# Performance work log

Measured on AMD Instinct MI355X. Metric: run time of the kernel, lower is better.

Reference implementation:

```python
import jax, jax.numpy as jnp
import numpy as np

C = 1.0          # Poincare ball curvature
H = 8            # num_heads
EPS = 1e-15
DELTA = 1e-7
SC = np.sqrt(C)  # sqrt curvature


def _norm(x):
    return jnp.sqrt(jnp.clip(jnp.sum(x * x, -1, keepdims=True), 1e-15))


def mobius_add(x, y):
    xy = jnp.sum(x * y, -1, keepdims=True)
    x2 = jnp.sum(x * x, -1, keepdims=True)
    y2 = jnp.sum(y * y, -1, keepdims=True)
    num = (1 + 2 * C * xy + C * y2) * x + (1 - C * x2) * y
    den = 1 + 2 * C * xy + C * C * x2 * y2
    return num / (den + EPS)


def mobius_matvec(W, x):
    xn = _norm(x)
    mx = x @ W.T
    mxn = _norm(mx)
    arg = jnp.clip(SC * xn, None, 1 - 1e-5)
    return jnp.tanh(mxn / xn * jnp.arctanh(arg)) * mx / (mxn * SC)


def logmap0(x):
    xn = _norm(x)
    return jnp.arctanh(jnp.clip(SC * xn, None, 1 - 1e-5)) * x / (SC * xn)


def expmap0(u):
    un = _norm(u)
    return jnp.tanh(SC * un) * u / (SC * un)


def hyp_linear(W, b, x):
    return mobius_add(mobius_matvec(W, x), b)


def setup_inputs() -> dict:
    key = jax.random.key(0)
    ks = jax.random.split(key, 5)
    B, S, E = 2, 512, 256
    x = jax.random.normal(ks[0], (B, S, E), jnp.float32) * 0.02  # inside unit ball
    scale = float(np.sqrt(6.0 / (E + E)))  # xavier uniform bound
    Wq = jax.random.uniform(ks[1], (E, E), jnp.float32, -scale, scale)
    Wk = jax.random.uniform(ks[2], (E, E), jnp.float32, -scale, scale)
    Wv = jax.random.uniform(ks[3], (E, E), jnp.float32, -scale, scale)
    Wo = jax.random.uniform(ks[4], (E, E), jnp.float32, -scale, scale)
    z = jnp.zeros((E,), jnp.float32)
    head_scaling = jnp.ones((H, 1, 1), jnp.float32)
    return {"x": x, "Wq": Wq, "bq": z, "Wk": Wk, "bk": z, "Wv": Wv, "bv": z,
            "Wo": Wo, "bo": z, "head_scaling": head_scaling}


def reference(x, Wq, bq, Wk, bk, Wv, bv, Wo, bo, head_scaling):
    B, S, E = x.shape
    D = E // H
    q = hyp_linear(Wq, bq, x).reshape(B, S, H, D).transpose(0, 2, 1, 3)  # (B,H,S,D)
    k = hyp_linear(Wk, bk, x).reshape(B, S, H, D).transpose(0, 2, 1, 3)
    v = hyp_linear(Wv, bv, x).reshape(B, S, H, D).transpose(0, 2, 1, 3)
    max_norm = (1 - 1e-5) / SC
    q = jnp.minimum(q, max_norm)  # elementwise clamp_max, faithful to source
    k = jnp.minimum(k, max_norm)
    qn = C * jnp.sum(q * q, -1)[..., :, None]   # (B,H,Sq,1)
    kn = C * jnp.sum(k * k, -1)[..., None, :]   # (B,H,1,Sk)
    # pairwise mobius_add(-k, q): (B,H,Sq,Sk,D)
    diff = mobius_add(-k[:, :, None, :, :], q[:, :, :, None, :])
    dn = C * jnp.sum(diff * diff, -1)           # (B,H,Sq,Sk)
    denom = (1 - qn) * (1 - kn) + EPS
    a = jnp.maximum(1 + 2 * dn / denom, 1 + DELTA)
    dist = jnp.log(a + jnp.sqrt(a * a - 1))     # acosh
    scores = -dist / (head_scaling * np.sqrt(D))
    w = jax.nn.softmax(scores, -1)
    out = expmap0(jnp.einsum('bhqk,bhkd->bhqd', w, logmap0(v)))
    out = out.transpose(0, 2, 1, 3).reshape(B, S, E)
    return hyp_linear(Wo, bo, out)
```

## Files before the change

kernel.cpp:

```cpp
#include <hip/hip_runtime.h>
#include <math.h>

#define Ec 256
#define Sc 512
#define Bc 2
#define Hc 8
#define Dc 32
#define MAXNORM (1.0f - 1e-5f)
#define NEc (Bc * Sc * Ec)

__device__ __forceinline__ float fullWaveSum(float v) {
#pragma unroll
  for (int m = 32; m >= 1; m >>= 1) v += __shfl_xor(v, m, 64);
  return v;
}
__device__ __forceinline__ float halfWaveSum(float v) {
#pragma unroll
  for (int m = 16; m >= 1; m >>= 1) v += __shfl_xor(v, m, 64);
  return v;
}
__device__ __forceinline__ float atanh_fast(float z) {
  return 0.5f * __logf((1.0f + z) / (1.0f - z));
}
__device__ __forceinline__ float tanh_fast(float a) {
  float e = __expf(-2.0f * a);
  return (1.0f - e) / (1.0f + e);
}

__global__ __launch_bounds__(128) void gemm_xwt(
    const float* __restrict__ X,
    const float* __restrict__ W0, const float* __restrict__ W1,
    const float* __restrict__ W2,
    float* __restrict__ O0, float* __restrict__ O1, float* __restrict__ O2) {
  const int tid = threadIdx.x;
  const int bx = blockIdx.x;
  const int by = blockIdx.y;
  const int kz = blockIdx.z;
  const int mat = by >> 2;
  const int cb0 = (by & 3) * 64;
  const int rb0 = bx * 32;
  const float* __restrict__ W = (mat == 0) ? W0 : (mat == 1) ? W1 : W2;
  float* __restrict__ O = ((mat == 0) ? O0 : (mat == 1) ? O1 : O2) + (size_t)kz * NEc;

  __shared__ float Xs[64][36];
  __shared__ float Ws[64][68];

  const int f4 = tid & 15;
  const int sub = tid >> 4;
  const int ty = tid >> 4;
  const int tx = tid & 15;

  float acc[4][4];
#pragma unroll
  for (int i = 0; i < 4; ++i)
#pragma unroll
    for (int j = 0; j < 4; ++j) acc[i][j] = 0.f;

  for (int kk = kz * 128; kk < kz * 128 + 128; kk += 64) {
    __syncthreads();
#pragma unroll
    for (int i = 0; i < 4; ++i) {
      int row = sub + i * 8;
      float4 v = *(const float4*)&X[(size_t)(rb0 + row) * Ec + kk + f4 * 4];
      Xs[f4 * 4 + 0][row] = v.x;
      Xs[f4 * 4 + 1][row] = v.y;
      Xs[f4 * 4 + 2][row] = v.z;
      Xs[f4 * 4 + 3][row] = v.w;
    }
#pragma unroll
    for (int i = 0; i < 8; ++i) {
      int col = sub + i * 8;
      float4 v = *(const float4*)&W[(size_t)(cb0 + col) * Ec + kk + f4 * 4];
      Ws[f4 * 4 + 0][col] = v.x;
      Ws[f4 * 4 + 1][col] = v.y;
      Ws[f4 * 4 + 2][col] = v.z;
      Ws[f4 * 4 + 3][col] = v.w;
    }
    __syncthreads();
#pragma unroll 8
    for (int k = 0; k < 64; ++k) {
      float4 a = *(const float4*)&Xs[k][ty * 4];
      float4 b = *(const float4*)&Ws[k][tx * 4];
      float av[4] = {a.x, a.y, a.z, a.w};
      float bv[4] = {b.x, b.y, b.z, b.w};
#pragma unroll
      for (int i = 0; i < 4; ++i)
#pragma unroll
        for (int j = 0; j < 4; ++j) acc[i][j] = fmaf(av[i], bv[j], acc[i][j]);
    }
  }
#pragma unroll
  for (int i = 0; i < 4; ++i) {
    float4 o = make_float4(acc[i][0], acc[i][1], acc[i][2], acc[i][3]);
    *(float4*)&O[(size_t)(rb0 + ty * 4 + i) * Ec + cb0 + tx * 4] = o;
  }
}

__global__ __launch_bounds__(256) void qkv_stats(
    const float* __restrict__ x,
    const float* __restrict__ mxq, const float* __restrict__ mxk,
    const float* __restrict__ mxv,
    const float* __restrict__ bq, const float* __restrict__ bk,
    const float* __restrict__ bv,
    float* __restrict__ qo, float* __restrict__ ko, float* __restrict__ lvo,
    float* __restrict__ qno, float* __restrict__ kno) {
  const int t = threadIdx.x;
  const int row = blockIdx.x;
  const int b = row >> 9;
  const int s = row & (Sc - 1);
  const size_t idx = (size_t)row * Ec + t;
  const float xv = x[idx];
  const float mq = mxq[idx] + mxq[idx + NEc];
  const float mk = mxk[idx] + mxk[idx + NEc];
  const float mv = mxv[idx] + mxv[idx + NEc];
  const float bb[3] = {bq[t], bk[t], bv[t]};
  const float mvals[3] = {mq, mk, mv};

  float vals[10] = {xv * xv,
                    mq * mq, mq * bb[0], bb[0] * bb[0],
                    mk * mk, mk * bb[1], bb[1] * bb[1],
                    mv * mv, mv * bb[2], bb[2] * bb[2]};
  __shared__ float red[10][4];
  __shared__ float fin[10];
#pragma unroll
  for (int i = 0; i < 10; ++i) {
    float v = fullWaveSum(vals[i]);
    if ((t & 63) == 0) red[i][t >> 6] = v;
  }
  __syncthreads();
  if (t < 10) fin[t] = red[t][0] + red[t][1] + red[t][2] + red[t][3];
  __syncthreads();

  const float x2 = fin[0];
  const float xn = sqrtf(fmaxf(x2, 1e-15f));
  const float at = atanh_fast(fminf(xn, MAXNORM));
  const int h = t >> 5;

#pragma unroll
  for (int m = 0; m < 3; ++m) {
    float mx2 = fin[1 + 3 * m];
    float mxb = fin[2 + 3 * m];
    float b2 = fin[3 + 3 * m];
    float mxn = sqrtf(fmaxf(mx2, 1e-15f));
    float scl = tanh_fast((mxn / xn) * at) / mxn;
    float mvv = scl * mvals[m];
    float X2 = scl * scl * mx2;
    float XY = scl * mxb;
    float numc = 1.0f + 2.0f * XY + b2;
    float den = 1.0f + 2.0f * XY + X2 * b2 + 1e-15f;
    float res = (numc * mvv + (1.0f - X2) * bb[m]) / den;
    if (m < 2) {
      res = fminf(res, MAXNORM);
      float s2 = halfWaveSum(res * res);
      if (m == 0) {
        qo[idx] = res;
        if ((t & 31) == 0) qno[(b * Hc + h) * Sc + s] = s2;
      } else {
        ko[idx] = res;
        if ((t & 31) == 0) kno[(b * Hc + h) * Sc + s] = s2;
      }
    } else {
      float vn2 = halfWaveSum(res * res);
      float vn = sqrtf(fmaxf(vn2, 1e-15f));
      float f = atanh_fast(fminf(vn, MAXNORM)) / vn;
      lvo[idx] = f * res;
    }
  }
}

__global__ __launch_bounds__(256, 2) void attn_kernel(
    const float* __restrict__ q, const float* __restrict__ k,
    const float* __restrict__ lv, const float* __restrict__ qn,
    const float* __restrict__ kn, const float* __restrict__ hs,
    float* __restrict__ out) {
  const int tid = threadIdx.x;
  const int rs = tid & 7;
  const int g = tid >> 3;
  const int blk = blockIdx.x;
  const int qt = blk & 31;
  const int h = (blk >> 5) & 7;
  const int b = blk >> 8;
  const int sq0 = qt * 16 + rs;

  const float* q0p = q + (size_t)(b * Sc + sq0) * Ec + h * Dc;
  const float* q1p = q0p + 8 * Ec;
  float4 qv0[8], qv1[8];
#pragma unroll
  for (int i = 0; i < 8; ++i) {
    qv0[i] = ((const float4*)q0p)[i];
    qv1[i] = ((const float4*)q1p)[i];
  }
  const float q20 = qn[(b * Hc + h) * Sc + sq0];
  const float q21 = qn[(b * Hc + h) * Sc + sq0 + 8];
  const float opq0 = 1.0f + q20, opq1 = 1.0f + q21;
  const float omq0 = 1.0f - q20, omq1 = 1.0f - q21;
  const float sinv = -1.0f / (hs[h] * sqrtf((float)Dc));

  const float* kbp = k + (size_t)(b * Sc) * Ec + h * Dc;
  const float* lvp = lv + (size_t)(b * Sc) * Ec + h * Dc;
  const float* knp = kn + (b * Hc + h) * Sc;

  float4 acc0[8], acc1[8];
#pragma unroll
  for (int i = 0; i < 8; ++i) {
    acc0[i] = make_float4(0.f, 0.f, 0.f, 0.f);
    acc1[i] = make_float4(0.f, 0.f, 0.f, 0.f);
  }
  float l0 = 0.f, l1 = 0.f;

#pragma unroll 1
  for (int jj = 0; jj < 16; ++jj) {
    const int j = g * 16 + jj;
    const float4* kr = (const float4*)(kbp + (size_t)j * Ec);
    const float4* lr = (const float4*)(lvp + (size_t)j * Ec);
    float4 kv[8], lvv[8];
#pragma unroll
    for (int i = 0; i < 8; ++i) kv[i] = kr[i];
    const float k2 = knp[j];
#pragma unroll
    for (int i = 0; i < 8; ++i) lvv[i] = lr[i];

    float kq0 = 0.f, kq1 = 0.f;
#pragma unroll
    for (int i = 0; i < 8; ++i) {
      kq0 = fmaf(qv0[i].x, kv[i].x, kq0);
      kq0 = fmaf(qv0[i].y, kv[i].y, kq0);
      kq0 = fmaf(qv0[i].z, kv[i].z, kq0);
      kq0 = fmaf(qv0[i].w, kv[i].w, kq0);
      kq1 = fmaf(qv1[i].x, kv[i].x, kq1);
      kq1 = fmaf(qv1[i].y, kv[i].y, kq1);
      kq1 = fmaf(qv1[i].z, kv[i].z, kq1);
      kq1 = fmaf(qv1[i].w, kv[i].w, kq1);
    }
    const float omk = 1.0f - k2;

    float A = fmaf(-2.0f, kq0, opq0);
    float dden = fmaf(k2, q20, fmaf(-2.0f, kq0, 1.0f)) + 1e-15f;
    float di = __builtin_amdgcn_rcpf(dden);
    float num2 = fmaf(A * A, k2, fmaf(-2.0f * A * omk, kq0, omk * omk * q20));
    float dn = num2 * di * di;
    float rd = __builtin_amdgcn_rcpf(fmaf(omq0, omk, 1e-15f));
    float tt = fmaxf(2.0f * dn * rd, 1e-7f);
    float z = 1.0f + tt + sqrtf(fmaf(tt, tt, 2.0f * tt));
    float p0 = __expf(sinv * __logf(z));
    A = fmaf(-2.0f, kq1, opq1);
    dden = fmaf(k2, q21, fmaf(-2.0f, kq1, 1.0f)) + 1e-15f;
    di = __builtin_amdgcn_rcpf(dden);
    num2 = fmaf(A * A, k2, fmaf(-2.0f * A * omk, kq1, omk * omk * q21));
    dn = num2 * di * di;
    rd = __builtin_amdgcn_rcpf(fmaf(omq1, omk, 1e-15f));
    tt = fmaxf(2.0f * dn * rd, 1e-7f);
    z = 1.0f + tt + sqrtf(fmaf(tt, tt, 2.0f * tt));
    float p1 = __expf(sinv * __logf(z));

    l0 += p0;
    l1 += p1;
#pragma unroll
    for (int i = 0; i < 8; ++i) {
      acc0[i].x = fmaf(p0, lvv[i].x, acc0[i].x);
      acc0[i].y = fmaf(p0, lvv[i].y, acc0[i].y);
      acc0[i].z = fmaf(p0, lvv[i].z, acc0[i].z);
      acc0[i].w = fmaf(p0, lvv[i].w, acc0[i].w);
      acc1[i].x = fmaf(p1, lvv[i].x, acc1[i].x);
      acc1[i].y = fmaf(p1, lvv[i].y, acc1[i].y);
      acc1[i].z = fmaf(p1, lvv[i].z, acc1[i].z);
      acc1[i].w = fmaf(p1, lvv[i].w, acc1[i].w);
    }
  }

  __shared__ float accb[32][8][36];
  __shared__ float lsb[32][8];
  const int mr = tid >> 5;
  const int md = tid & 31;
  const size_t obase = (size_t)(b * Sc + qt * 16) * Ec + h * Dc + md;

#pragma unroll 1
  for (int chunk = 0; chunk < 2; ++chunk) {
    float* ap = &accb[g][rs][0];
#pragma unroll
    for (int i = 0; i < 8; ++i)
      ((float4*)ap)[i] = chunk ? acc1[i] : acc0[i];
    lsb[g][rs] = chunk ? l1 : l0;
    __syncthreads();

    float osum = 0.f, lsum = 0.f;
#pragma unroll
    for (int gg = 0; gg < 32; ++gg) {
      osum += accb[gg][mr][md];
      lsum += lsb[gg][mr];
    }
    float o = osum / lsum;
    float un2 = o * o;
#pragma unroll
    for (int m = 16; m >= 1; m >>= 1) un2 += __shfl_xor(un2, m, 32);
    float un = sqrtf(fmaxf(un2, 1e-15f));
    float f = tanh_fast(un) / un;
    out[obase + (size_t)(chunk * 8 + mr) * Ec] = o * f;
    __syncthreads();
  }
}

__global__ __launch_bounds__(256) void proj_stats(
    const float* __restrict__ xin, const float* __restrict__ mx,
    const float* __restrict__ bo, float* __restrict__ out) {
  const int t = threadIdx.x;
  const int row = blockIdx.x;
  const size_t idx = (size_t)row * Ec + t;
  const float xv = xin[idx];
  const float m = mx[idx] + mx[idx + NEc];
  const float bb = bo[t];
  float vals[4] = {xv * xv, m * m, m * bb, bb * bb};
  __shared__ float red[4][4];
  __shared__ float fin[4];
#pragma unroll
  for (int i = 0; i < 4; ++i) {
    float v = fullWaveSum(vals[i]);
    if ((t & 63) == 0) red[i][t >> 6] = v;
  }
  __syncthreads();
  if (t < 4) fin[t] = red[t][0] + red[t][1] + red[t][2] + red[t][3];
  __syncthreads();

  float x2 = fin[0], mx2 = fin[1], mxb = fin[2], b2 = fin[3];
  float xn = sqrtf(fmaxf(x2, 1e-15f));
  float mxn = sqrtf(fmaxf(mx2, 1e-15f));
  float scl = tanh_fast((mxn / xn) * atanh_fast(fminf(xn, MAXNORM))) / mxn;
  float mvv = scl * m;
  float X2 = scl * scl * mx2;
  float XY = scl * mxb;
  float numc = 1.0f + 2.0f * XY + b2;
  float den = 1.0f + 2.0f * XY + X2 * b2 + 1e-15f;
  out[idx] = (numc * mvv + (1.0f - X2) * bb) / den;
}

extern "C" void kernel_launch(void* const* d_in, const int* in_sizes, int n_in,
                              void* d_out, int out_size, void* d_ws, size_t ws_size,
                              hipStream_t stream) {
  (void)in_sizes; (void)n_in; (void)out_size; (void)ws_size;
  const float* x  = (const float*)d_in[0];
  const float* Wq = (const float*)d_in[1];
  const float* bq = (const float*)d_in[2];
  const float* Wk = (const float*)d_in[3];
  const float* bk = (const float*)d_in[4];
  const float* Wv = (const float*)d_in[5];
  const float* bv = (const float*)d_in[6];
  const float* Wo = (const float*)d_in[7];
  const float* bo = (const float*)d_in[8];
  const float* hs = (const float*)d_in[9];

  float* ws = (float*)d_ws;
  const int NE = NEc;
  const int NH = Bc * Hc * Sc;
  float* mxq = ws;
  float* mxk = mxq + 2 * NE;
  float* mxv = mxk + 2 * NE;
  float* qb  = mxv + 2 * NE;
  float* kb  = qb + NE;
  float* lvb = kb + NE;
  float* qnb = lvb + NE;
  float* knb = qnb + NH;
  float* aob = knb + NH;
  float* mxo = aob + NE;

  const int M = Bc * Sc;

  gemm_xwt<<<dim3(M / 32, 12, 2), 128, 0, stream>>>(x, Wq, Wk, Wv, mxq, mxk, mxv);
  qkv_stats<<<M, 256, 0, stream>>>(x, mxq, mxk, mxv, bq, bk, bv,
                                   qb, kb, lvb, qnb, knb);
  attn_kernel<<<512, 256, 0, stream>>>(qb, kb, lvb, qnb, knb, hs, aob);
  gemm_xwt<<<dim3(M / 32, 4, 2), 128, 0, stream>>>(aob, Wo, Wo, Wo, mxo, mxo, mxo);
  proj_stats<<<M, 256, 0, stream>>>(aob, mxo, bo, (float*)d_out);
}
```

Before: 145.8 us.

## Increase GEMM split-K to four and halve query rows per attention block

The projection GEMMs now split K four ways (one 64-wide tile per block), and the stats kernels sum four partials instead of two. The attention kernel handles one query row per thread instead of two, doubling the grid to 1024 blocks, dropping the min-2-waves launch bound, and reducing across key groups with a two-stage shared-memory pass. The aim is more parallelism and lower register pressure. In exchange, K/V rows are reloaded by twice as many blocks, and the larger split-K partial buffers add workspace traffic.

Result: faster. 142.7 us (-2.1%).

```diff
diff --git a/kernel.cpp b/kernel.cpp
--- a/kernel.cpp
+++ b/kernel.cpp
@@ -8,6 +8,7 @@
 #define Dc 32
 #define MAXNORM (1.0f - 1e-5f)
 #define NEc (Bc * Sc * Ec)
+#define KSPLIT 4
 
 __device__ __forceinline__ float fullWaveSum(float v) {
 #pragma unroll
@@ -39,6 +40,7 @@
   const int mat = by >> 2;
   const int cb0 = (by & 3) * 64;
   const int rb0 = bx * 32;
+  const int kk = kz * 64;
   const float* __restrict__ W = (mat == 0) ? W0 : (mat == 1) ? W1 : W2;
   float* __restrict__ O = ((mat == 0) ? O0 : (mat == 1) ? O1 : O2) + (size_t)kz * NEc;
 
@@ -50,44 +52,42 @@
   const int ty = tid >> 4;
   const int tx = tid & 15;
 
+#pragma unroll
+  for (int i = 0; i < 4; ++i) {
+    int row = sub + i * 8;
+    float4 v = *(const float4*)&X[(size_t)(rb0 + row) * Ec + kk + f4 * 4];
+    Xs[f4 * 4 + 0][row] = v.x;
+    Xs[f4 * 4 + 1][row] = v.y;
+    Xs[f4 * 4 + 2][row] = v.z;
+    Xs[f4 * 4 + 3][row] = v.w;
+  }
+#pragma unroll
+  for (int i = 0; i < 8; ++i) {
+    int col = sub + i * 8;
+    float4 v = *(const float4*)&W[(size_t)(cb0 + col) * Ec + kk + f4 * 4];
+    Ws[f4 * 4 + 0][col] = v.x;
+    Ws[f4 * 4 + 1][col] = v.y;
+    Ws[f4 * 4 + 2][col] = v.z;
+    Ws[f4 * 4 + 3][col] = v.w;
+  }
+  __syncthreads();
+
   float acc[4][4];
 #pragma unroll
   for (int i = 0; i < 4; ++i)
 #pragma unroll
     for (int j = 0; j < 4; ++j) acc[i][j] = 0.f;
 
-  for (int kk = kz * 128; kk < kz * 128 + 128; kk += 64) {
-    __syncthreads();
-#pragma unroll
-    for (int i = 0; i < 4; ++i) {
-      int row = sub + i * 8;
-      float4 v = *(const float4*)&X[(size_t)(rb0 + row) * Ec + kk + f4 * 4];
-      Xs[f4 * 4 + 0][row] = v.x;
-      Xs[f4 * 4 + 1][row] = v.y;
-      Xs[f4 * 4 + 2][row] = v.z;
-      Xs[f4 * 4 + 3][row] = v.w;
-    }
-#pragma unroll
-    for (int i = 0; i < 8; ++i) {
-      int col = sub + i * 8;
-      float4 v = *(const float4*)&W[(size_t)(cb0 + col) * Ec + kk + f4 * 4];
-      Ws[f4 * 4 + 0][col] = v.x;
-      Ws[f4 * 4 + 1][col] = v.y;
-      Ws[f4 * 4 + 2][col] = v.z;
-      Ws[f4 * 4 + 3][col] = v.w;
-    }
-    __syncthreads();
 #pragma unroll 8
-    for (int k = 0; k < 64; ++k) {
-      float4 a = *(const float4*)&Xs[k][ty * 4];
-      float4 b = *(const float4*)&Ws[k][tx * 4];
-      float av[4] = {a.x, a.y, a.z, a.w};
-      float bv[4] = {b.x, b.y, b.z, b.w};
-#pragma unroll
-      for (int i = 0; i < 4; ++i)
-#pragma unroll
-        for (int j = 0; j < 4; ++j) acc[i][j] = fmaf(av[i], bv[j], acc[i][j]);
-    }
+  for (int k = 0; k < 64; ++k) {
+    float4 a = *(const float4*)&Xs[k][ty * 4];
+    float4 b = *(const float4*)&Ws[k][tx * 4];
+    float av[4] = {a.x, a.y, a.z, a.w};
+    float bv[4] = {b.x, b.y, b.z, b.w};
+#pragma unroll
+    for (int i = 0; i < 4; ++i)
+#pragma unroll
+      for (int j = 0; j < 4; ++j) acc[i][j] = fmaf(av[i], bv[j], acc[i][j]);
   }
 #pragma unroll
   for (int i = 0; i < 4; ++i) {
@@ -110,9 +110,13 @@
   const int s = row & (Sc - 1);
   const size_t idx = (size_t)row * Ec + t;
   const float xv = x[idx];
-  const float mq = mxq[idx] + mxq[idx + NEc];
-  const float mk = mxk[idx] + mxk[idx + NEc];
-  const float mv = mxv[idx] + mxv[idx + NEc];
+  float mq = 0.f, mk = 0.f, mv = 0.f;
+#pragma unroll
+  for (int p = 0; p < KSPLIT; ++p) {
+    mq += mxq[idx + (size_t)p * NEc];
+    mk += mxk[idx + (size_t)p * NEc];
+    mv += mxv[idx + (size_t)p * NEc];
+  }
   const float bb[3] = {bq[t], bk[t], bv[t]};
   const float mvals[3] = {mq, mk, mv};
 
@@ -168,7 +172,7 @@
   }
 }
 
-__global__ __launch_bounds__(256, 2) void attn_kernel(
+__global__ __launch_bounds__(256) void attn_kernel(
     const float* __restrict__ q, const float* __restrict__ k,
     const float* __restrict__ lv, const float* __restrict__ qn,
     const float* __restrict__ kn, const float* __restrict__ hs,
@@ -177,127 +181,106 @@
   const int rs = tid & 7;
   const int g = tid >> 3;
   const int blk = blockIdx.x;
-  const int qt = blk & 31;
-  const int h = (blk >> 5) & 7;
-  const int b = blk >> 8;
-  const int sq0 = qt * 16 + rs;
-
-  const float* q0p = q + (size_t)(b * Sc + sq0) * Ec + h * Dc;
-  const float* q1p = q0p + 8 * Ec;
-  float4 qv0[8], qv1[8];
-#pragma unroll
-  for (int i = 0; i < 8; ++i) {
-    qv0[i] = ((const float4*)q0p)[i];
-    qv1[i] = ((const float4*)q1p)[i];
-  }
-  const float q20 = qn[(b * Hc + h) * Sc + sq0];
-  const float q21 = qn[(b * Hc + h) * Sc + sq0 + 8];
-  const float opq0 = 1.0f + q20, opq1 = 1.0f + q21;
-  const float omq0 = 1.0f - q20, omq1 = 1.0f - q21;
+  const int qt = blk & 63;
+  const int h = (blk >> 6) & 7;
+  const int b = blk >> 9;
+  const int sq = qt * 8 + rs;
+
+  const float* qrow = q + (size_t)(b * Sc + sq) * Ec + h * Dc;
+  float4 qv[8];
+#pragma unroll
+  for (int i = 0; i < 8; ++i) qv[i] = ((const float4*)qrow)[i];
+  const float q2 = qn[(b * Hc + h) * Sc + sq];
+  const float opq = 1.0f + q2;
+  const float omq = 1.0f - q2;
   const float sinv = -1.0f / (hs[h] * sqrtf((float)Dc));
 
   const float* kbp = k + (size_t)(b * Sc) * Ec + h * Dc;
   const float* lvp = lv + (size_t)(b * Sc) * Ec + h * Dc;
   const float* knp = kn + (b * Hc + h) * Sc;
 
-  float4 acc0[8], acc1[8];
-#pragma unroll
-  for (int i = 0; i < 8; ++i) {
-    acc0[i] = make_float4(0.f, 0.f, 0.f, 0.f);
-    acc1[i] = make_float4(0.f, 0.f, 0.f, 0.f);
-  }
-  float l0 = 0.f, l1 = 0.f;
+  float4 acc[8];
+#pragma unroll
+  for (int i = 0; i < 8; ++i) acc[i] = make_float4(0.f, 0.f, 0.f, 0.f);
+  float l = 0.f;
 
 #pragma unroll 1
   for (int jj = 0; jj < 16; ++jj) {
     const int j = g * 16 + jj;
     const float4* kr = (const float4*)(kbp + (size_t)j * Ec);
-    const float4* lr = (const float4*)(lvp + (size_t)j * Ec);
-    float4 kv[8], lvv[8];
+    float4 kv[8];
 #pragma unroll
     for (int i = 0; i < 8; ++i) kv[i] = kr[i];
     const float k2 = knp[j];
-#pragma unroll
-    for (int i = 0; i < 8; ++i) lvv[i] = lr[i];
-
-    float kq0 = 0.f, kq1 = 0.f;
+
+    float kq = 0.f;
 #pragma unroll
     for (int i = 0; i < 8; ++i) {
-      kq0 = fmaf(qv0[i].x, kv[i].x, kq0);
-      kq0 = fmaf(qv0[i].y, kv[i].y, kq0);
-      kq0 = fmaf(qv0[i].z, kv[i].z, kq0);
-      kq0 = fmaf(qv0[i].w, kv[i].w, kq0);
-      kq1 = fmaf(qv1[i].x, kv[i].x, kq1);
-      kq1 = fmaf(qv1[i].y, kv[i].y, kq1);
-      kq1 = fmaf(qv1[i].z, kv[i].z, kq1);
-      kq1 = fmaf(qv1[i].w, kv[i].w, kq1);
+      kq = fmaf(qv[i].x, kv[i].x, kq);
+      kq = fmaf(qv[i].y, kv[i].y, kq);
+      kq = fmaf(qv[i].z, kv[i].z, kq);
+      kq = fmaf(qv[i].w, kv[i].w, kq);
     }
     const float omk = 1.0f - k2;
-
-    float A = fmaf(-2.0f, kq0, opq0);
-    float dden = fmaf(k2, q20, fmaf(-2.0f, kq0, 1.0f)) + 1e-15f;
+    float A = fmaf(-2.0f, kq, opq);
+    float dden = fmaf(k2, q2, fmaf(-2.0f, kq, 1.0f)) + 1e-15f;
     float di = __builtin_amdgcn_rcpf(dden);
-    float num2 = fmaf(A * A, k2, fmaf(-2.0f * A * omk, kq0, omk * omk * q20));
+    float num2 = fmaf(A * A, k2, fmaf(-2.0f * A * omk, kq, omk * omk * q2));
     float dn = num2 * di * di;
-    float rd = __builtin_amdgcn_rcpf(fmaf(omq0, omk, 1e-15f));
+    float rd = __builtin_amdgcn_rcpf(fmaf(omq, omk, 1e-15f));
     float tt = fmaxf(2.0f * dn * rd, 1e-7f);
     float z = 1.0f + tt + sqrtf(fmaf(tt, tt, 2.0f * tt));
-    float p0 = __expf(sinv * __logf(z));
-    A = fmaf(-2.0f, kq1, opq1);
-    dden = fmaf(k2, q21, fmaf(-2.0f, kq1, 1.0f)) + 1e-15f;
-    di = __builtin_amdgcn_rcpf(dden);
-    num2 = fmaf(A * A, k2, fmaf(-2.0f * A * omk, kq1, omk * omk * q21));
-    dn = num2 * di * di;
-    rd = __builtin_amdgcn_rcpf(fmaf(omq1, omk, 1e-15f));
-    tt = fmaxf(2.0f * dn * rd, 1e-7f);
-    z = 1.0f + tt + sqrtf(fmaf(tt, tt, 2.0f * tt));
-    float p1 = __expf(sinv * __logf(z));
-
-    l0 += p0;
-    l1 += p1;
+    float p = __expf(sinv * __logf(z));
+    l += p;
+
+    const float4* lr = (const float4*)(lvp + (size_t)j * Ec);
 #pragma unroll
     for (int i = 0; i < 8; ++i) {
-      acc0[i].x = fmaf(p0, lvv[i].x, acc0[i].x);
-      acc0[i].y = fmaf(p0, lvv[i].y, acc0[i].y);
-      acc0[i].z = fmaf(p0, lvv[i].z, acc0[i].z);
-      acc0[i].w = fmaf(p0, lvv[i].w, acc0[i].w);
-      acc1[i].x = fmaf(p1, lvv[i].x, acc1[i].x);
-      acc1[i].y = fmaf(p1, lvv[i].y, acc1[i].y);
-      acc1[i].z = fmaf(p1, lvv[i].z, acc1[i].z);
-      acc1[i].w = fmaf(p1, lvv[i].w, acc1[i].w);
+      float4 lvv = lr[i];
+      acc[i].x = fmaf(p, lvv.x, acc[i].x);
+      acc[i].y = fmaf(p, lvv.y, acc[i].y);
+      acc[i].z = fmaf(p, lvv.z, acc[i].z);
+      acc[i].w = fmaf(p, lvv.w, acc[i].w);
     }
   }
 
-  __shared__ float accb[32][8][36];
-  __shared__ float lsb[32][8];
+  __shared__ float accb[16][8][36];
+  __shared__ float lsb[16][8];
+
+  if (g >= 16) {
+    float* ap = &accb[g - 16][rs][0];
+#pragma unroll
+    for (int i = 0; i < 8; ++i) ((float4*)ap)[i] = acc[i];
+    lsb[g - 16][rs] = l;
+  }
+  __syncthreads();
+  if (g < 16) {
+    float* ap = &accb[g][rs][0];
+#pragma unroll
+    for (int i = 0; i < 8; ++i) {
+      float4 t = ((float4*)ap)[i];
+      t.x += acc[i].x; t.y += acc[i].y; t.z += acc[i].z; t.w += acc[i].w;
+      ((float4*)ap)[i] = t;
+    }
+    lsb[g][rs] += l;
+  }
+  __syncthreads();
+
   const int mr = tid >> 5;
   const int md = tid & 31;
-  const size_t obase = (size_t)(b * Sc + qt * 16) * Ec + h * Dc + md;
-
-#pragma unroll 1
-  for (int chunk = 0; chunk < 2; ++chunk) {
-    float* ap = &accb[g][rs][0];
-#pragma unroll
-    for (int i = 0; i < 8; ++i)
-      ((float4*)ap)[i] = chunk ? acc1[i] : acc0[i];
-    lsb[g][rs] = chunk ? l1 : l0;
-    __syncthreads();
-
-    float osum = 0.f, lsum = 0.f;
-#pragma unroll
-    for (int gg = 0; gg < 32; ++gg) {
-      osum += accb[gg][mr][md];
-      lsum += lsb[gg][mr];
-    }
-    float o = osum / lsum;
-    float un2 = o * o;
-#pragma unroll
-    for (int m = 16; m >= 1; m >>= 1) un2 += __shfl_xor(un2, m, 32);
-    float un = sqrtf(fmaxf(un2, 1e-15f));
-    float f = tanh_fast(un) / un;
-    out[obase + (size_t)(chunk * 8 + mr) * Ec] = o * f;
-    __syncthreads();
-  }
+  float osum = 0.f, lsum = 0.f;
+#pragma unroll
+  for (int gg = 0; gg < 16; ++gg) {
+    osum += accb[gg][mr][md];
+    lsum += lsb[gg][mr];
+  }
+  float o = osum / lsum;
+  float un2 = o * o;
+#pragma unroll
+  for (int m = 16; m >= 1; m >>= 1) un2 += __shfl_xor(un2, m, 32);
+  float un = sqrtf(fmaxf(un2, 1e-15f));
+  float f = tanh_fast(un) / un;
+  out[(size_t)(b * Sc + qt * 8 + mr) * Ec + h * Dc + md] = o * f;
 }
 
 __global__ __launch_bounds__(256) void proj_stats(
@@ -307,7 +290,9 @@
   const int row = blockIdx.x;
   const size_t idx = (size_t)row * Ec + t;
   const float xv = xin[idx];
-  const float m = mx[idx] + mx[idx + NEc];
+  float m = 0.f;
+#pragma unroll
+  for (int p = 0; p < KSPLIT; ++p) m += mx[idx + (size_t)p * NEc];
   const float bb = bo[t];
   float vals[4] = {xv * xv, m * m, m * bb, bb * bb};
   __shared__ float red[4][4];
@@ -352,22 +337,22 @@
   const int NE = NEc;
   const int NH = Bc * Hc * Sc;
   float* mxq = ws;
-  float* mxk = mxq + 2 * NE;
-  float* mxv = mxk + 2 * NE;
-  float* qb  = mxv + 2 * NE;
+  float* mxk = mxq + KSPLIT * NE;
+  float* mxv = mxk + KSPLIT * NE;
+  float* mxo = mxv + KSPLIT * NE;
+  float* qb  = mxo + KSPLIT * NE;
   float* kb  = qb + NE;
   float* lvb = kb + NE;
-  float* qnb = lvb + NE;
+  float* aob = lvb + NE;
+  float* qnb = aob + NE;
   float* knb = qnb + NH;
-  float* aob = knb + NH;
-  float* mxo = aob + NE;
 
   const int M = Bc * Sc;
 
-  gemm_xwt<<<dim3(M / 32, 12, 2), 128, 0, stream>>>(x, Wq, Wk, Wv, mxq, mxk, mxv);
+  gemm_xwt<<<dim3(M / 32, 12, KSPLIT), 128, 0, stream>>>(x, Wq, Wk, Wv, mxq, mxk, mxv);
   qkv_stats<<<M, 256, 0, stream>>>(x, mxq, mxk, mxv, bq, bk, bv,
                                    qb, kb, lvb, qnb, knb);
-  attn_kernel<<<512, 256, 0, stream>>>(qb, kb, lvb, qnb, knb, hs, aob);
-  gemm_xwt<<<dim3(M / 32, 4, 2), 128, 0, stream>>>(aob, Wo, Wo, Wo, mxo, mxo, mxo);
+  attn_kernel<<<1024, 256, 0, stream>>>(qb, kb, lvb, qnb, knb, hs, aob);
+  gemm_xwt<<<dim3(M / 32, 4, KSPLIT), 128, 0, stream>>>(aob, Wo, Wo, Wo, mxo, mxo, mxo);
   proj_stats<<<M, 256, 0, stream>>>(aob, mxo, bo, (float*)d_out);
 }
```
